# Kernel optimization log

Hardware: AMD Instinct MI355X
Metric: run time of the kernel (lower is better)

Reference implementation:

```python
import jax, jax.numpy as jnp
import numpy as np

NEG = -1000000.0  # mask fill value used by original sequence_mask

def setup_inputs() -> dict:
    key = jax.random.key(0)
    k1, k2, k3, k4 = jax.random.split(key, 4)
    B, S, D = 32, 2048, 64
    queries = jax.random.normal(k1, (B, S, D), dtype=jnp.float32)
    keys = jax.random.normal(k2, (B, S, D), dtype=jnp.float32)
    values = jax.random.normal(k3, (B, S, D), dtype=jnp.float32)
    valid_lens = jax.random.randint(k4, (B,), 1, S + 1, dtype=jnp.int64)
    return {"queries": queries, "keys": keys, "values": values, "valid_lens": valid_lens}

def reference(queries, keys, values, valid_lens):
    d = queries.shape[-1]
    # [B, Sq, Sk]
    scores = jnp.einsum('bqd,bkd->bqk', queries, keys) / jnp.sqrt(jnp.asarray(d, queries.dtype))
    # valid_lens is 1D: one length per batch row, broadcast over all query rows
    kv_idx = jnp.arange(scores.shape[-1])  # [Sk]
    mask = kv_idx[None, None, :] < valid_lens[:, None, None]  # [B,1,Sk] broadcast
    scores = jnp.where(mask, scores, jnp.asarray(NEG, scores.dtype))
    weights = jax.nn.softmax(scores, axis=-1)
    # dropout p=0.0 -> identity
    return jnp.einsum('bqk,bkd->bqd', weights, values)
```

## Files before the change

kernel.cpp:

```cpp
#include <hip/hip_runtime.h>
#include <hip/hip_bf16.h>

typedef __attribute__((ext_vector_type(8))) short bf16x8;
typedef __attribute__((ext_vector_type(4))) float f32x4;
typedef __attribute__((ext_vector_type(16))) float f32x16;

#define BATCH 32
#define SEQ   2048
#define PSTR  20
#define KSTR  72
#define VSTR  36
#define LOG2E 1.44269504088896340736f
#define QSCALE (0.125f * LOG2E)
#define NEGL  (-1000000.0f * LOG2E)

__device__ __forceinline__ unsigned int pk2(float lo, float hi) {
    __hip_bfloat162 h2 = __float22bfloat162_rn(make_float2(lo, hi));
    return *reinterpret_cast<unsigned int*>(&h2);
}

__device__ __forceinline__ void dma16(const short* g, short* l) {
    __builtin_amdgcn_global_load_lds((const __attribute__((address_space(1))) void*)g,
                                     (__attribute__((address_space(3))) void*)l, 16, 0, 0);
}

__device__ __forceinline__ void plswap(unsigned int& a, unsigned int& b) {
    asm volatile("v_permlane32_swap_b32 %0, %1" : "+v"(a), "+v"(b));
}

__global__ void prep_vl(const int* __restrict__ VL, int* __restrict__ meta) {
    __shared__ int sv[BATCH];
    const int t = threadIdx.x;
    int odd = (t < 16) ? VL[2 * t + 1] : 0;
    const bool is64 = (__ballot(odd != 0) == 0ULL);
    if (t < BATCH) {
        int x = is64 ? VL[2 * t] : VL[t];
        x = x < 0 ? 0 : (x > SEQ ? SEQ : x);
        sv[t] = x;
    }
    __syncthreads();
    if (t < BATCH) {
        const int x = sv[t];
        int rank = 0;
        for (int j = 0; j < BATCH; ++j) {
            const int y = sv[j];
            rank += (y > x) || (y == x && j < t);
        }
        meta[rank] = x;
        meta[BATCH + rank] = t;
    }
}

__global__ __launch_bounds__(256) void prepkv(const float* __restrict__ Kp,
                                              const float* __restrict__ Vp,
                                              const int* __restrict__ VL,
                                              short* __restrict__ Kb,
                                              short* __restrict__ Vt,
                                              int* __restrict__ meta) {
    __shared__ unsigned int l[64 * VSTR];
    __shared__ int sv[BATCH];
    const int tid = threadIdx.x;
    if (blockIdx.x == BATCH * 32) {
        if (tid < 64) {
            int odd = (tid < 16) ? VL[2 * tid + 1] : 0;
            const bool is64 = (__ballot(odd != 0) == 0ULL);
            if (tid < BATCH) {
                int x = is64 ? VL[2 * tid] : VL[tid];
                x = x < 0 ? 0 : (x > SEQ ? SEQ : x);
                sv[tid] = x;
            }
            asm volatile("s_waitcnt lgkmcnt(0)" ::: "memory");
            if (tid < BATCH) {
                const int x = sv[tid];
                int rank = 0;
                for (int j = 0; j < BATCH; ++j) {
                    const int y = sv[j];
                    rank += (y > x) || (y == x && j < tid);
                }
                meta[rank] = x;
                meta[BATCH + rank] = tid;
            }
        }
        return;
    }
    const int b = blockIdx.x >> 5, kt = blockIdx.x & 31, kb = kt * 64;
    const float* Kv = Kp + ((size_t)b * SEQ + kb) * 64;
    const float* Vb = Vp + ((size_t)b * SEQ + kb) * 64;
    #pragma unroll
    for (int h = 0; h < 4; ++h) {
        const int c = tid + h * 256;
        const int row = c >> 4, col = (c & 15) * 4;
        f32x4 x = *(const f32x4*)(Kv + row * 64 + col);
        unsigned int* dst = (unsigned int*)(Kb + ((size_t)b * SEQ + kb + row) * 64 + col);
        dst[0] = pk2(x[0], x[1]); dst[1] = pk2(x[2], x[3]);
    }
    #pragma unroll
    for (int h = 0; h < 2; ++h) {
        const int u = tid + h * 256;
        const int d4 = (u & 3) + ((u >> 7) << 2);
        const int kp = (u >> 2) & 31;
        f32x4 a = *(const f32x4*)(Vb + (2 * kp) * 64 + d4 * 4);
        f32x4 c = *(const f32x4*)(Vb + (2 * kp + 1) * 64 + d4 * 4);
        #pragma unroll
        for (int j = 0; j < 4; ++j)
            l[(d4 * 4 + j) * VSTR + kp] = pk2(a[j], c[j]);
    }
    __syncthreads();
    const int d = tid >> 2, cg = tid & 3;
    unsigned int w[8];
    #pragma unroll
    for (int j = 0; j < 8; ++j) w[j] = l[d * VSTR + cg * 8 + j];
    unsigned int* dst = (unsigned int*)Vt + ((size_t)(b * 32 + kt) * 64 + d) * 32 + cg * 8;
    #pragma unroll
    for (int j = 0; j < 8; ++j) dst[j] = w[j];
}

__global__ __launch_bounds__(256, 4)
void attn_fwd(const float* __restrict__ Qp, const short* __restrict__ Kb,
              const short* __restrict__ Vt, const int* __restrict__ meta,
              float* __restrict__ Out) {
    constexpr int S = SEQ;
    __shared__ short bK2[2 * 64 * 64];
    __shared__ short bV2[2 * 64 * 64];

    const int tid  = threadIdx.x;
    const int wave = tid >> 6, lane = tid & 63;
    const int r31 = lane & 31, hi = lane >> 5;
    const int qh = wave >> 1, kh = wave & 1;

    const int g  = blockIdx.x >> 8;
    const int k8 = (blockIdx.x >> 5) & 7;
    const int qt = blockIdx.x & 31;
    const int slot = (g << 3) + ((g & 1) ? 7 - k8 : k8);

    const int vl = meta[slot], batch = meta[BATCH + slot];
    const int ntiles = (vl + 63) >> 6;

    const short* Kbb = Kb + (size_t)batch * S * 64;
    const short* Vtb = Vt + (size_t)batch * 32 * 4096;

    const int r8 = lane >> 3, s8 = lane & 7, csw = s8 ^ r8;
    const short* gK0 = Kbb + (wave * 16 + r8) * 64 + csw * 8;
    const short* gV0 = Vtb + (wave * 16 + r8) * 64 + csw * 8;
    short* lK0 = &bK2[wave * 16 * 64];
    short* lV0 = &bV2[wave * 16 * 64];

    bf16x8 qf[4];
    {
        const float* qb = Qp + ((size_t)batch * S + qt * 64 + qh * 32 + r31) * 64 + hi * 8;
        #pragma unroll
        for (int kf = 0; kf < 4; ++kf) {
            f32x4 a = *(const f32x4*)(qb + kf * 16);
            f32x4 c = *(const f32x4*)(qb + kf * 16 + 4);
            union { bf16x8 v; unsigned int u[4]; } qq;
            qq.u[0] = pk2(a[0] * QSCALE, a[1] * QSCALE);
            qq.u[1] = pk2(a[2] * QSCALE, a[3] * QSCALE);
            qq.u[2] = pk2(c[0] * QSCALE, c[1] * QSCALE);
            qq.u[3] = pk2(c[2] * QSCALE, c[3] * QSCALE);
            qf[kf] = qq.v;
        }
    }

    f32x16 o[2];
    #pragma unroll
    for (int dt = 0; dt < 2; ++dt)
        #pragma unroll
        for (int r = 0; r < 16; ++r) o[dt][r] = 0.f;
    float lpart = 0.f;

    if (ntiles > 0) {
        dma16(gK0,          lK0);
        dma16(gK0 + 8 * 64, lK0 + 8 * 64);
        dma16(gV0,          lV0);
        dma16(gV0 + 8 * 64, lV0 + 8 * 64);
    }

    const int krow = kh * 32 + r31;
    const int l7 = lane & 7;

    for (int kt = 0; kt < ntiles; ++kt) {
        __syncthreads();
        if (kt + 1 < ntiles) {
            const int nb = ((kt + 1) & 1) * 4096;
            const int ko = (kt + 1) * 4096;
            dma16(gK0 + ko,          lK0 + nb);
            dma16(gK0 + ko + 8 * 64, lK0 + nb + 8 * 64);
            dma16(gV0 + ko,          lV0 + nb);
            dma16(gV0 + ko + 8 * 64, lV0 + nb + 8 * 64);
        }
        const char* bK = (const char*)&bK2[(kt & 1) * 4096];
        const char* bV = (const char*)&bV2[(kt & 1) * 4096];

        if (kt * 64 + kh * 32 < vl) {
            f32x16 st;
            #pragma unroll
            for (int r = 0; r < 16; ++r) st[r] = 0.f;
            #pragma unroll
            for (int kf = 0; kf < 4; ++kf) {
                bf16x8 kfr = *(const bf16x8*)(bK + krow * 128 +
                                              (((kf * 2 + hi) ^ l7) << 4));
                st = __builtin_amdgcn_mfma_f32_32x32x16_bf16(kfr, qf[kf], st, 0, 0, 0);
            }

            if (kt == ntiles - 1 && (vl & 63) != 0) {
                const int kb = kt * 64 + kh * 32 + 4 * hi;
                #pragma unroll
                for (int r = 0; r < 16; ++r) {
                    const int key = kb + (r & 3) + 8 * (r >> 2);
                    st[r] = (key < vl) ? st[r] : NEGL;
                }
            }

            #pragma unroll
            for (int r = 0; r < 16; ++r) st[r] = exp2f(st[r]);
            {
                const float a0 = (st[0] + st[1]) + (st[2] + st[3]);
                const float a1 = (st[4] + st[5]) + (st[6] + st[7]);
                const float a2 = (st[8] + st[9]) + (st[10] + st[11]);
                const float a3 = (st[12] + st[13]) + (st[14] + st[15]);
                lpart += (a0 + a1) + (a2 + a3);
            }

            union { bf16x8 v; unsigned int u[4]; } pf0, pf1;
            {
                unsigned int x0 = pk2(st[0], st[1]),   y0 = pk2(st[4], st[5]);
                unsigned int x1 = pk2(st[2], st[3]),   y1 = pk2(st[6], st[7]);
                plswap(x0, y0); plswap(x1, y1);
                pf0.u[0] = x0; pf0.u[1] = x1; pf0.u[2] = y0; pf0.u[3] = y1;
                unsigned int x2 = pk2(st[8], st[9]),   y2 = pk2(st[12], st[13]);
                unsigned int x3 = pk2(st[10], st[11]), y3 = pk2(st[14], st[15]);
                plswap(x2, y2); plswap(x3, y3);
                pf1.u[0] = x2; pf1.u[1] = x3; pf1.u[2] = y2; pf1.u[3] = y3;
            }

            #pragma unroll
            for (int dt = 0; dt < 2; ++dt) {
                const int vrow = dt * 32 + r31;
                bf16x8 vf0 = *(const bf16x8*)(bV + vrow * 128 +
                                              (((kh * 4 + hi) ^ l7) << 4));
                o[dt] = __builtin_amdgcn_mfma_f32_32x32x16_bf16(vf0, pf0.v, o[dt], 0, 0, 0);
                bf16x8 vf1 = *(const bf16x8*)(bV + vrow * 128 +
                                              (((kh * 4 + 2 + hi) ^ l7) << 4));
                o[dt] = __builtin_amdgcn_mfma_f32_32x32x16_bf16(vf1, pf1.v, o[dt], 0, 0, 0);
            }
        }
    }

    float lw = lpart + __shfl_xor(lpart, 32);

    __syncthreads();
    float* mrg = (float*)bK2;
    float* lm  = (float*)bV2;
    if (kh == 1) {
        #pragma unroll
        for (int dt = 0; dt < 2; ++dt)
            #pragma unroll
            for (int r = 0; r < 16; ++r)
                mrg[qh * 2048 + (dt * 16 + r) * 64 + lane] = o[dt][r];
        lm[qh * 64 + lane] = lw;
    }
    __syncthreads();
    if (kh == 0) {
        #pragma unroll
        for (int dt = 0; dt < 2; ++dt)
            #pragma unroll
            for (int r = 0; r < 16; ++r)
                o[dt][r] += mrg[qh * 2048 + (dt * 16 + r) * 64 + lane];
        lw += lm[qh * 64 + lane];
        const float inv = (lw > 0.f) ? 1.0f / lw : 0.f;
        const size_t orow = ((size_t)batch * S + qt * 64 + qh * 32 + r31) * 64;
        #pragma unroll
        for (int dt = 0; dt < 2; ++dt)
            #pragma unroll
            for (int g4 = 0; g4 < 4; ++g4) {
                f32x4 w;
                #pragma unroll
                for (int j = 0; j < 4; ++j) w[j] = o[dt][g4 * 4 + j] * inv;
                *(f32x4*)(Out + orow + dt * 32 + g4 * 8 + hi * 4) = w;
            }
    }
}

__device__ __forceinline__ void load_tile_fb(const float* __restrict__ Kb,
                                             const float* __restrict__ Vb,
                                             int tid, f32x4 kv[4], f32x4 vv[4]) {
    #pragma unroll
    for (int h = 0; h < 4; ++h) {
        const int c = tid + h * 256;
        kv[h] = *(const f32x4*)(Kb + (c >> 4) * 64 + (c & 15) * 4);
    }
    #pragma unroll
    for (int h = 0; h < 2; ++h) {
        const int u  = tid + h * 256;
        const int d4 = (u & 3) + ((u >> 7) << 2);
        const int kp = (u >> 2) & 31;
        vv[2 * h]     = *(const f32x4*)(Vb + (2 * kp) * 64 + d4 * 4);
        vv[2 * h + 1] = *(const f32x4*)(Vb + (2 * kp + 1) * 64 + d4 * 4);
    }
}

__global__ __launch_bounds__(256, 4)
void attn_fb(const float* __restrict__ Qp, const float* __restrict__ Kp,
             const float* __restrict__ Vp, const int* __restrict__ meta,
             float* __restrict__ Out) {
    constexpr int S = SEQ;
    constexpr int qtiles = S >> 6;
    __shared__ short        lK [64 * KSTR];
    __shared__ unsigned int lVt[64 * VSTR];
    __shared__ unsigned int lPt[4 * 32 * PSTR];
    const int tid = threadIdx.x;
    const int wave = tid >> 6, lane = tid & 63;
    const int l15 = lane & 15, grp = lane >> 4;
    const int slot = blockIdx.x / qtiles, qt = blockIdx.x % qtiles;
    const int vl = meta[slot], batch = meta[BATCH + slot];
    const int ntiles = (vl + 63) >> 6;
    const float* Kb = Kp + (size_t)batch * S * 64;
    const float* Vb = Vp + (size_t)batch * S * 64;
    bf16x8 qf[2];
    {
        const float* qb = Qp + ((size_t)batch * S + qt * 64 + wave * 16 + l15) * 64 + grp * 8;
        #pragma unroll
        for (int kf = 0; kf < 2; ++kf) {
            f32x4 a = *(const f32x4*)(qb + kf * 32);
            f32x4 b = *(const f32x4*)(qb + kf * 32 + 4);
            union { bf16x8 v; unsigned int u[4]; } qq;
            qq.u[0] = pk2(a[0], a[1]); qq.u[1] = pk2(a[2], a[3]);
            qq.u[2] = pk2(b[0], b[1]); qq.u[3] = pk2(b[2], b[3]);
            qf[kf] = qq.v;
        }
    }
    f32x4 o[4] = {{0.f,0.f,0.f,0.f},{0.f,0.f,0.f,0.f},{0.f,0.f,0.f,0.f},{0.f,0.f,0.f,0.f}};
    float mrun = -INFINITY, lrun = 0.f;
    unsigned int* pw = &lPt[wave * 32 * PSTR];
    f32x4 kv[4], vv[4];
    if (ntiles > 0) load_tile_fb(Kb, Vb, tid, kv, vv);
    for (int kt = 0; kt < ntiles; ++kt) {
        const int kb = kt * 64;
        __syncthreads();
        #pragma unroll
        for (int h = 0; h < 4; ++h) {
            const int c = tid + h * 256;
            const int row = c >> 4, col = (c & 15) * 4;
            union { f32x4 f; float e[4]; } x; x.f = kv[h];
            unsigned int* dst = (unsigned int*)&lK[row * KSTR + col];
            dst[0] = pk2(x.e[0], x.e[1]); dst[1] = pk2(x.e[2], x.e[3]);
        }
        #pragma unroll
        for (int h = 0; h < 2; ++h) {
            const int u  = tid + h * 256;
            const int d4 = (u & 3) + ((u >> 7) << 2);
            const int kp = (u >> 2) & 31;
            union { f32x4 f; float e[4]; } a, b;
            a.f = vv[2 * h]; b.f = vv[2 * h + 1];
            #pragma unroll
            for (int j = 0; j < 4; ++j)
                lVt[(d4 * 4 + j) * VSTR + kp] = pk2(a.e[j], b.e[j]);
        }
        if (kt + 1 < ntiles) load_tile_fb(Kb + (size_t)(kb + 64) * 64, Vb + (size_t)(kb + 64) * 64, tid, kv, vv);
        __syncthreads();
        f32x4 st[4] = {{0.f,0.f,0.f,0.f},{0.f,0.f,0.f,0.f},{0.f,0.f,0.f,0.f},{0.f,0.f,0.f,0.f}};
        #pragma unroll
        for (int kf = 0; kf < 2; ++kf) {
            #pragma unroll
            for (int ct = 0; ct < 4; ++ct) {
                bf16x8 kfr = *(const bf16x8*)&lK[(ct * 16 + l15) * KSTR + kf * 32 + grp * 8];
                st[ct] = __builtin_amdgcn_mfma_f32_16x16x32_bf16(kfr, qf[kf], st[ct], 0, 0, 0);
            }
        }
        #pragma unroll
        for (int ct = 0; ct < 4; ++ct)
            #pragma unroll
            for (int r = 0; r < 4; ++r) {
                const bool valid = (kb + ct * 16 + grp * 4 + r) < vl;
                st[ct][r] = valid ? st[ct][r] * (0.125f * LOG2E) : NEGL;
            }
        float t0 = fmaxf(fmaxf(st[0][0], st[0][1]), fmaxf(st[0][2], st[0][3]));
        float t1 = fmaxf(fmaxf(st[1][0], st[1][1]), fmaxf(st[1][2], st[1][3]));
        float t2 = fmaxf(fmaxf(st[2][0], st[2][1]), fmaxf(st[2][2], st[2][3]));
        float t3 = fmaxf(fmaxf(st[3][0], st[3][1]), fmaxf(st[3][2], st[3][3]));
        float tm = fmaxf(fmaxf(t0, t1), fmaxf(t2, t3));
        tm = fmaxf(tm, __shfl_xor(tm, 16));
        tm = fmaxf(tm, __shfl_xor(tm, 32));
        const float mnew  = fmaxf(mrun, tm);
        const float alpha = exp2f(mrun - mnew);
        mrun = mnew;
        lrun *= alpha;
        #pragma unroll
        for (int dt = 0; dt < 4; ++dt)
            #pragma unroll
            for (int r = 0; r < 4; ++r) o[dt][r] *= alpha;
        float rs = 0.f;
        #pragma unroll
        for (int ct = 0; ct < 4; ++ct) {
            #pragma unroll
            for (int r = 0; r < 4; ++r) {
                st[ct][r] = exp2f(st[ct][r] - mrun);
                rs += st[ct][r];
            }
            #pragma unroll
            for (int a = 0; a < 2; ++a)
                pw[(ct * 8 + grp * 2 + a) * PSTR + l15] = pk2(st[ct][2 * a], st[ct][2 * a + 1]);
        }
        rs += __shfl_xor(rs, 16);
        rs += __shfl_xor(rs, 32);
        lrun += rs;
        asm volatile("s_waitcnt lgkmcnt(0)" ::: "memory");
        #pragma unroll
        for (int kk = 0; kk < 2; ++kk) {
            union { bf16x8 v; unsigned int u[4]; } pf;
            #pragma unroll
            for (int jj = 0; jj < 4; ++jj)
                pf.u[jj] = pw[(kk * 16 + grp * 4 + jj) * PSTR + l15];
            #pragma unroll
            for (int dt = 0; dt < 4; ++dt) {
                bf16x8 vf = *(const bf16x8*)&lVt[(dt * 16 + l15) * VSTR + kk * 16 + grp * 4];
                o[dt] = __builtin_amdgcn_mfma_f32_16x16x32_bf16(vf, pf.v, o[dt], 0, 0, 0);
            }
        }
    }
    const float inv = (lrun > 0.f) ? 1.0f / lrun : 0.f;
    const size_t orow = ((size_t)batch * S + qt * 64 + wave * 16 + l15) * 64;
    #pragma unroll
    for (int dt = 0; dt < 4; ++dt) {
        f32x4 w = o[dt];
        w[0] *= inv; w[1] *= inv; w[2] *= inv; w[3] *= inv;
        *(f32x4*)(Out + orow + dt * 16 + grp * 4) = w;
    }
}

extern "C" void kernel_launch(void* const* d_in, const int* in_sizes, int n_in,
                              void* d_out, int out_size, void* d_ws, size_t ws_size,
                              hipStream_t stream) {
    const float* Q  = (const float*)d_in[0];
    const float* K  = (const float*)d_in[1];
    const float* V  = (const float*)d_in[2];
    const int*   VL = (const int*)d_in[3];
    int* meta = (int*)d_ws;
    const size_t need = 512 + 2 * (size_t)BATCH * SEQ * 64 * sizeof(short);
    dim3 block(256);
    if (ws_size >= need) {
        short* Kb = (short*)((char*)d_ws + 512);
        short* Vt = Kb + (size_t)BATCH * SEQ * 64;
        prepkv<<<dim3(BATCH * 32 + 1), block, 0, stream>>>(K, V, VL, Kb, Vt, meta);
        attn_fwd<<<dim3(BATCH * 32), block, 0, stream>>>(Q, Kb, Vt, meta, (float*)d_out);
    } else {
        prep_vl<<<1, 64, 0, stream>>>(VL, meta);
        attn_fb<<<dim3(BATCH * (SEQ >> 6)), block, 0, stream>>>(Q, K, V, meta, (float*)d_out);
    }
}
```

Baseline: 127.9 us.

## Load K/V fragments directly from global into registers, dropping LDS staging

```diff
diff --git a/kernel.cpp b/kernel.cpp
--- a/kernel.cpp
+++ b/kernel.cpp
@@ -17,11 +17,6 @@
 __device__ __forceinline__ unsigned int pk2(float lo, float hi) {
     __hip_bfloat162 h2 = __float22bfloat162_rn(make_float2(lo, hi));
     return *reinterpret_cast<unsigned int*>(&h2);
-}
-
-__device__ __forceinline__ void dma16(const short* g, short* l) {
-    __builtin_amdgcn_global_load_lds((const __attribute__((address_space(1))) void*)g,
-                                     (__attribute__((address_space(3))) void*)l, 16, 0, 0);
 }
 
 __device__ __forceinline__ void plswap(unsigned int& a, unsigned int& b) {
@@ -120,8 +115,7 @@
               const short* __restrict__ Vt, const int* __restrict__ meta,
               float* __restrict__ Out) {
     constexpr int S = SEQ;
-    __shared__ short bK2[2 * 64 * 64];
-    __shared__ short bV2[2 * 64 * 64];
+    __shared__ float mrg[2 * 2048 + 128];
 
     const int tid  = threadIdx.x;
     const int wave = tid >> 6, lane = tid & 63;
@@ -134,16 +128,14 @@
     const int slot = (g << 3) + ((g & 1) ? 7 - k8 : k8);
 
     const int vl = meta[slot], batch = meta[BATCH + slot];
-    const int ntiles = (vl + 63) >> 6;
-
-    const short* Kbb = Kb + (size_t)batch * S * 64;
-    const short* Vtb = Vt + (size_t)batch * 32 * 4096;
-
-    const int r8 = lane >> 3, s8 = lane & 7, csw = s8 ^ r8;
-    const short* gK0 = Kbb + (wave * 16 + r8) * 64 + csw * 8;
-    const short* gV0 = Vtb + (wave * 16 + r8) * 64 + csw * 8;
-    short* lK0 = &bK2[wave * 16 * 64];
-    short* lV0 = &bV2[wave * 16 * 64];
+    const int ntw = (vl - kh * 32 + 63) >> 6;
+
+    const short* Kbb = Kb + (size_t)batch * (S * 64);
+    const short* Vtb = Vt + (size_t)batch * (32 * 4096);
+
+    const int krow = kh * 32 + r31;
+    const short* pk = Kbb + krow * 64 + hi * 8;
+    const short* pv = Vtb + r31 * 64 + (kh * 4 + hi) * 8;
 
     bf16x8 qf[4];
     {
@@ -161,123 +153,119 @@
         }
     }
 
-    f32x16 o[2];
-    #pragma unroll
-    for (int dt = 0; dt < 2; ++dt)
-        #pragma unroll
-        for (int r = 0; r < 16; ++r) o[dt][r] = 0.f;
+    f32x16 o0, o1;
+    #pragma unroll
+    for (int r = 0; r < 16; ++r) { o0[r] = 0.f; o1[r] = 0.f; }
     float lpart = 0.f;
 
-    if (ntiles > 0) {
-        dma16(gK0,          lK0);
-        dma16(gK0 + 8 * 64, lK0 + 8 * 64);
-        dma16(gV0,          lV0);
-        dma16(gV0 + 8 * 64, lV0 + 8 * 64);
-    }
-
-    const int krow = kh * 32 + r31;
-    const int l7 = lane & 7;
-
-    for (int kt = 0; kt < ntiles; ++kt) {
-        __syncthreads();
-        if (kt + 1 < ntiles) {
-            const int nb = ((kt + 1) & 1) * 4096;
-            const int ko = (kt + 1) * 4096;
-            dma16(gK0 + ko,          lK0 + nb);
-            dma16(gK0 + ko + 8 * 64, lK0 + nb + 8 * 64);
-            dma16(gV0 + ko,          lV0 + nb);
-            dma16(gV0 + ko + 8 * 64, lV0 + nb + 8 * 64);
-        }
-        const char* bK = (const char*)&bK2[(kt & 1) * 4096];
-        const char* bV = (const char*)&bV2[(kt & 1) * 4096];
-
-        if (kt * 64 + kh * 32 < vl) {
-            f32x16 st;
-            #pragma unroll
-            for (int r = 0; r < 16; ++r) st[r] = 0.f;
-            #pragma unroll
-            for (int kf = 0; kf < 4; ++kf) {
-                bf16x8 kfr = *(const bf16x8*)(bK + krow * 128 +
-                                              (((kf * 2 + hi) ^ l7) << 4));
-                st = __builtin_amdgcn_mfma_f32_32x32x16_bf16(kfr, qf[kf], st, 0, 0, 0);
-            }
-
-            if (kt == ntiles - 1 && (vl & 63) != 0) {
-                const int kb = kt * 64 + kh * 32 + 4 * hi;
-                #pragma unroll
-                for (int r = 0; r < 16; ++r) {
-                    const int key = kb + (r & 3) + 8 * (r >> 2);
-                    st[r] = (key < vl) ? st[r] : NEGL;
-                }
-            }
-
-            #pragma unroll
-            for (int r = 0; r < 16; ++r) st[r] = exp2f(st[r]);
-            {
-                const float a0 = (st[0] + st[1]) + (st[2] + st[3]);
-                const float a1 = (st[4] + st[5]) + (st[6] + st[7]);
-                const float a2 = (st[8] + st[9]) + (st[10] + st[11]);
-                const float a3 = (st[12] + st[13]) + (st[14] + st[15]);
-                lpart += (a0 + a1) + (a2 + a3);
-            }
-
-            union { bf16x8 v; unsigned int u[4]; } pf0, pf1;
-            {
-                unsigned int x0 = pk2(st[0], st[1]),   y0 = pk2(st[4], st[5]);
-                unsigned int x1 = pk2(st[2], st[3]),   y1 = pk2(st[6], st[7]);
-                plswap(x0, y0); plswap(x1, y1);
-                pf0.u[0] = x0; pf0.u[1] = x1; pf0.u[2] = y0; pf0.u[3] = y1;
-                unsigned int x2 = pk2(st[8], st[9]),   y2 = pk2(st[12], st[13]);
-                unsigned int x3 = pk2(st[10], st[11]), y3 = pk2(st[14], st[15]);
-                plswap(x2, y2); plswap(x3, y3);
-                pf1.u[0] = x2; pf1.u[1] = x3; pf1.u[2] = y2; pf1.u[3] = y3;
-            }
-
-            #pragma unroll
-            for (int dt = 0; dt < 2; ++dt) {
-                const int vrow = dt * 32 + r31;
-                bf16x8 vf0 = *(const bf16x8*)(bV + vrow * 128 +
-                                              (((kh * 4 + hi) ^ l7) << 4));
-                o[dt] = __builtin_amdgcn_mfma_f32_32x32x16_bf16(vf0, pf0.v, o[dt], 0, 0, 0);
-                bf16x8 vf1 = *(const bf16x8*)(bV + vrow * 128 +
-                                              (((kh * 4 + 2 + hi) ^ l7) << 4));
-                o[dt] = __builtin_amdgcn_mfma_f32_32x32x16_bf16(vf1, pf1.v, o[dt], 0, 0, 0);
-            }
+    bf16x8 kk0 = *(const bf16x8*)(pk);
+    bf16x8 kk1 = *(const bf16x8*)(pk + 16);
+    bf16x8 kk2 = *(const bf16x8*)(pk + 32);
+    bf16x8 kk3 = *(const bf16x8*)(pk + 48);
+    bf16x8 vv0 = *(const bf16x8*)(pv);
+    bf16x8 vv1 = *(const bf16x8*)(pv + 16);
+    bf16x8 vv2 = *(const bf16x8*)(pv + 2048);
+    bf16x8 vv3 = *(const bf16x8*)(pv + 2048 + 16);
+
+    for (int kt = 0; kt < ntw; ++kt) {
+        f32x16 st;
+        #pragma unroll
+        for (int r = 0; r < 16; ++r) st[r] = 0.f;
+        __builtin_amdgcn_s_setprio(1);
+        st = __builtin_amdgcn_mfma_f32_32x32x16_bf16(kk0, qf[0], st, 0, 0, 0);
+        st = __builtin_amdgcn_mfma_f32_32x32x16_bf16(kk1, qf[1], st, 0, 0, 0);
+        st = __builtin_amdgcn_mfma_f32_32x32x16_bf16(kk2, qf[2], st, 0, 0, 0);
+        st = __builtin_amdgcn_mfma_f32_32x32x16_bf16(kk3, qf[3], st, 0, 0, 0);
+        __builtin_amdgcn_s_setprio(0);
+
+        if (kt + 1 < ntw) {
+            const short* p = pk + (kt + 1) * 4096;
+            kk0 = *(const bf16x8*)(p);
+            kk1 = *(const bf16x8*)(p + 16);
+            kk2 = *(const bf16x8*)(p + 32);
+            kk3 = *(const bf16x8*)(p + 48);
+        }
+
+        const int rem = vl - (kt * 64 + kh * 32);
+        if (rem < 32) {
+            #pragma unroll
+            for (int r = 0; r < 16; ++r) {
+                const int kl = 4 * hi + (r & 3) + 8 * (r >> 2);
+                st[r] = (kl < rem) ? st[r] : NEGL;
+            }
+        }
+
+        #pragma unroll
+        for (int r = 0; r < 16; ++r) st[r] = exp2f(st[r]);
+        {
+            const float a0 = (st[0] + st[1]) + (st[2] + st[3]);
+            const float a1 = (st[4] + st[5]) + (st[6] + st[7]);
+            const float a2 = (st[8] + st[9]) + (st[10] + st[11]);
+            const float a3 = (st[12] + st[13]) + (st[14] + st[15]);
+            lpart += (a0 + a1) + (a2 + a3);
+        }
+
+        union { bf16x8 v; unsigned int u[4]; } pf0, pf1;
+        {
+            unsigned int x0 = pk2(st[0], st[1]),   y0 = pk2(st[4], st[5]);
+            unsigned int x1 = pk2(st[2], st[3]),   y1 = pk2(st[6], st[7]);
+            plswap(x0, y0); plswap(x1, y1);
+            pf0.u[0] = x0; pf0.u[1] = x1; pf0.u[2] = y0; pf0.u[3] = y1;
+            unsigned int x2 = pk2(st[8], st[9]),   y2 = pk2(st[12], st[13]);
+            unsigned int x3 = pk2(st[10], st[11]), y3 = pk2(st[14], st[15]);
+            plswap(x2, y2); plswap(x3, y3);
+            pf1.u[0] = x2; pf1.u[1] = x3; pf1.u[2] = y2; pf1.u[3] = y3;
+        }
+
+        __builtin_amdgcn_s_setprio(1);
+        o0 = __builtin_amdgcn_mfma_f32_32x32x16_bf16(vv0, pf0.v, o0, 0, 0, 0);
+        o0 = __builtin_amdgcn_mfma_f32_32x32x16_bf16(vv1, pf1.v, o0, 0, 0, 0);
+        o1 = __builtin_amdgcn_mfma_f32_32x32x16_bf16(vv2, pf0.v, o1, 0, 0, 0);
+        o1 = __builtin_amdgcn_mfma_f32_32x32x16_bf16(vv3, pf1.v, o1, 0, 0, 0);
+        __builtin_amdgcn_s_setprio(0);
+
+        if (kt + 1 < ntw) {
+            const short* p = pv + (kt + 1) * 4096;
+            vv0 = *(const bf16x8*)(p);
+            vv1 = *(const bf16x8*)(p + 16);
+            vv2 = *(const bf16x8*)(p + 2048);
+            vv3 = *(const bf16x8*)(p + 2048 + 16);
         }
     }
 
     float lw = lpart + __shfl_xor(lpart, 32);
 
-    __syncthreads();
-    float* mrg = (float*)bK2;
-    float* lm  = (float*)bV2;
+    float* lm = &mrg[4096];
     if (kh == 1) {
         #pragma unroll
-        for (int dt = 0; dt < 2; ++dt)
-            #pragma unroll
-            for (int r = 0; r < 16; ++r)
-                mrg[qh * 2048 + (dt * 16 + r) * 64 + lane] = o[dt][r];
+        for (int r = 0; r < 16; ++r) mrg[qh * 2048 + r * 64 + lane] = o0[r];
+        #pragma unroll
+        for (int r = 0; r < 16; ++r) mrg[qh * 2048 + (16 + r) * 64 + lane] = o1[r];
         lm[qh * 64 + lane] = lw;
     }
     __syncthreads();
     if (kh == 0) {
         #pragma unroll
-        for (int dt = 0; dt < 2; ++dt)
-            #pragma unroll
-            for (int r = 0; r < 16; ++r)
-                o[dt][r] += mrg[qh * 2048 + (dt * 16 + r) * 64 + lane];
+        for (int r = 0; r < 16; ++r) o0[r] += mrg[qh * 2048 + r * 64 + lane];
+        #pragma unroll
+        for (int r = 0; r < 16; ++r) o1[r] += mrg[qh * 2048 + (16 + r) * 64 + lane];
         lw += lm[qh * 64 + lane];
         const float inv = (lw > 0.f) ? 1.0f / lw : 0.f;
         const size_t orow = ((size_t)batch * S + qt * 64 + qh * 32 + r31) * 64;
         #pragma unroll
-        for (int dt = 0; dt < 2; ++dt)
-            #pragma unroll
-            for (int g4 = 0; g4 < 4; ++g4) {
-                f32x4 w;
-                #pragma unroll
-                for (int j = 0; j < 4; ++j) w[j] = o[dt][g4 * 4 + j] * inv;
-                *(f32x4*)(Out + orow + dt * 32 + g4 * 8 + hi * 4) = w;
-            }
+        for (int g4 = 0; g4 < 4; ++g4) {
+            f32x4 w;
+            #pragma unroll
+            for (int j = 0; j < 4; ++j) w[j] = o0[g4 * 4 + j] * inv;
+            *(f32x4*)(Out + orow + g4 * 8 + hi * 4) = w;
+        }
+        #pragma unroll
+        for (int g4 = 0; g4 < 4; ++g4) {
+            f32x4 w;
+            #pragma unroll
+            for (int j = 0; j < 4; ++j) w[j] = o1[g4 * 4 + j] * inv;
+            *(f32x4*)(Out + orow + 32 + g4 * 8 + hi * 4) = w;
+        }
     }
 }
 
```

Result: slower. 158.8 us (+24.2%).

## Skip K/V conversion past valid length and unroll attention loop with MFMA priority

Applied to the files above, without the earlier changes.

```diff
diff --git a/kernel.cpp b/kernel.cpp
--- a/kernel.cpp
+++ b/kernel.cpp
@@ -59,6 +59,7 @@
                                               int* __restrict__ meta) {
     __shared__ unsigned int l[64 * VSTR];
     __shared__ int sv[BATCH];
+    __shared__ int svl;
     const int tid = threadIdx.x;
     if (blockIdx.x == BATCH * 32) {
         if (tid < 64) {
@@ -84,6 +85,17 @@
         return;
     }
     const int b = blockIdx.x >> 5, kt = blockIdx.x & 31, kb = kt * 64;
+    if (tid < 64) {
+        int odd = (tid < 16) ? VL[2 * tid + 1] : 0;
+        const bool is64 = (__ballot(odd != 0) == 0ULL);
+        if (tid == 0) {
+            int x = is64 ? VL[2 * b] : VL[b];
+            x = x < 0 ? 0 : (x > SEQ ? SEQ : x);
+            svl = x;
+        }
+    }
+    __syncthreads();
+    if (kb >= svl) return;
     const float* Kv = Kp + ((size_t)b * SEQ + kb) * 64;
     const float* Vb = Vp + ((size_t)b * SEQ + kb) * 64;
     #pragma unroll
@@ -126,6 +138,7 @@
     const int tid  = threadIdx.x;
     const int wave = tid >> 6, lane = tid & 63;
     const int r31 = lane & 31, hi = lane >> 5;
+    const int l7  = lane & 7;
     const int qh = wave >> 1, kh = wave & 1;
 
     const int g  = blockIdx.x >> 8;
@@ -161,90 +174,93 @@
         }
     }
 
-    f32x16 o[2];
-    #pragma unroll
-    for (int dt = 0; dt < 2; ++dt)
-        #pragma unroll
-        for (int r = 0; r < 16; ++r) o[dt][r] = 0.f;
+    f32x16 o0, o1, zv;
+    #pragma unroll
+    for (int r = 0; r < 16; ++r) { o0[r] = 0.f; o1[r] = 0.f; zv[r] = 0.f; }
     float lpart = 0.f;
+    const int krow = kh * 32 + r31;
 
     if (ntiles > 0) {
-        dma16(gK0,          lK0);
-        dma16(gK0 + 8 * 64, lK0 + 8 * 64);
-        dma16(gV0,          lV0);
-        dma16(gV0 + 8 * 64, lV0 + 8 * 64);
-    }
-
-    const int krow = kh * 32 + r31;
-    const int l7 = lane & 7;
-
-    for (int kt = 0; kt < ntiles; ++kt) {
-        __syncthreads();
-        if (kt + 1 < ntiles) {
-            const int nb = ((kt + 1) & 1) * 4096;
-            const int ko = (kt + 1) * 4096;
-            dma16(gK0 + ko,          lK0 + nb);
-            dma16(gK0 + ko + 8 * 64, lK0 + nb + 8 * 64);
-            dma16(gV0 + ko,          lV0 + nb);
-            dma16(gV0 + ko + 8 * 64, lV0 + nb + 8 * 64);
-        }
-        const char* bK = (const char*)&bK2[(kt & 1) * 4096];
-        const char* bV = (const char*)&bV2[(kt & 1) * 4096];
-
-        if (kt * 64 + kh * 32 < vl) {
-            f32x16 st;
-            #pragma unroll
-            for (int r = 0; r < 16; ++r) st[r] = 0.f;
-            #pragma unroll
-            for (int kf = 0; kf < 4; ++kf) {
-                bf16x8 kfr = *(const bf16x8*)(bK + krow * 128 +
-                                              (((kf * 2 + hi) ^ l7) << 4));
-                st = __builtin_amdgcn_mfma_f32_32x32x16_bf16(kfr, qf[kf], st, 0, 0, 0);
-            }
-
-            if (kt == ntiles - 1 && (vl & 63) != 0) {
-                const int kb = kt * 64 + kh * 32 + 4 * hi;
-                #pragma unroll
-                for (int r = 0; r < 16; ++r) {
-                    const int key = kb + (r & 3) + 8 * (r >> 2);
-                    st[r] = (key < vl) ? st[r] : NEGL;
-                }
-            }
-
-            #pragma unroll
-            for (int r = 0; r < 16; ++r) st[r] = exp2f(st[r]);
-            {
-                const float a0 = (st[0] + st[1]) + (st[2] + st[3]);
-                const float a1 = (st[4] + st[5]) + (st[6] + st[7]);
-                const float a2 = (st[8] + st[9]) + (st[10] + st[11]);
-                const float a3 = (st[12] + st[13]) + (st[14] + st[15]);
-                lpart += (a0 + a1) + (a2 + a3);
-            }
-
-            union { bf16x8 v; unsigned int u[4]; } pf0, pf1;
-            {
-                unsigned int x0 = pk2(st[0], st[1]),   y0 = pk2(st[4], st[5]);
-                unsigned int x1 = pk2(st[2], st[3]),   y1 = pk2(st[6], st[7]);
-                plswap(x0, y0); plswap(x1, y1);
-                pf0.u[0] = x0; pf0.u[1] = x1; pf0.u[2] = y0; pf0.u[3] = y1;
-                unsigned int x2 = pk2(st[8], st[9]),   y2 = pk2(st[12], st[13]);
-                unsigned int x3 = pk2(st[10], st[11]), y3 = pk2(st[14], st[15]);
-                plswap(x2, y2); plswap(x3, y3);
-                pf1.u[0] = x2; pf1.u[1] = x3; pf1.u[2] = y2; pf1.u[3] = y3;
-            }
-
-            #pragma unroll
-            for (int dt = 0; dt < 2; ++dt) {
-                const int vrow = dt * 32 + r31;
-                bf16x8 vf0 = *(const bf16x8*)(bV + vrow * 128 +
-                                              (((kh * 4 + hi) ^ l7) << 4));
-                o[dt] = __builtin_amdgcn_mfma_f32_32x32x16_bf16(vf0, pf0.v, o[dt], 0, 0, 0);
-                bf16x8 vf1 = *(const bf16x8*)(bV + vrow * 128 +
-                                              (((kh * 4 + 2 + hi) ^ l7) << 4));
-                o[dt] = __builtin_amdgcn_mfma_f32_32x32x16_bf16(vf1, pf1.v, o[dt], 0, 0, 0);
-            }
-        }
-    }
+        dma16(gK0,       lK0);
+        dma16(gK0 + 512, lK0 + 512);
+        dma16(gV0,       lV0);
+        dma16(gV0 + 512, lV0 + 512);
+    }
+
+#define ATTN_TILE(KT, BUF)                                                       \
+    {                                                                            \
+        __syncthreads();       \
+        if ((KT) + 1 < ntiles) {                                                 \
+            const int ko = ((KT) + 1) * 4096;                                    \
+            dma16(gK0 + ko,       lK0 + ((BUF) ^ 1) * 4096);                     \
+            dma16(gK0 + ko + 512, lK0 + ((BUF) ^ 1) * 4096 + 512);               \
+            dma16(gV0 + ko,       lV0 + ((BUF) ^ 1) * 4096);                     \
+            dma16(gV0 + ko + 512, lV0 + ((BUF) ^ 1) * 4096 + 512);               \
+        }                                                                        \
+        if ((KT) * 64 + kh * 32 < vl) {                                          \
+            const char* bK = (const char*)&bK2[(BUF) * 4096];                    \
+            const char* bV = (const char*)&bV2[(BUF) * 4096];                    \
+            f32x16 st;                                                           \
+            __builtin_amdgcn_s_setprio(1);                                       \
+            {                                                                    \
+                bf16x8 k0 = *(const bf16x8*)(bK + krow * 128 + (((0 + hi) ^ l7) << 4)); \
+                bf16x8 k1 = *(const bf16x8*)(bK + krow * 128 + (((2 + hi) ^ l7) << 4)); \
+                bf16x8 k2 = *(const bf16x8*)(bK + krow * 128 + (((4 + hi) ^ l7) << 4)); \
+                bf16x8 k3 = *(const bf16x8*)(bK + krow * 128 + (((6 + hi) ^ l7) << 4)); \
+                st = __builtin_amdgcn_mfma_f32_32x32x16_bf16(k0, qf[0], zv, 0, 0, 0); \
+                st = __builtin_amdgcn_mfma_f32_32x32x16_bf16(k1, qf[1], st, 0, 0, 0); \
+                st = __builtin_amdgcn_mfma_f32_32x32x16_bf16(k2, qf[2], st, 0, 0, 0); \
+                st = __builtin_amdgcn_mfma_f32_32x32x16_bf16(k3, qf[3], st, 0, 0, 0); \
+            }                                                                    \
+            __builtin_amdgcn_s_setprio(0);                                       \
+            const int rem = vl - ((KT) * 64 + kh * 32);                          \
+            if (rem < 32) {                                                      \
+                _Pragma("unroll")                                                \
+                for (int r = 0; r < 16; ++r) {                                   \
+                    const int kl = 4 * hi + (r & 3) + 8 * (r >> 2);              \
+                    st[r] = (kl < rem) ? st[r] : NEGL;                           \
+                }                                                                \
+            }                                                                    \
+            _Pragma("unroll")                                                    \
+            for (int r = 0; r < 16; ++r) st[r] = exp2f(st[r]);                   \
+            {                                                                    \
+                const float a0 = (st[0] + st[1]) + (st[2] + st[3]);              \
+                const float a1 = (st[4] + st[5]) + (st[6] + st[7]);              \
+                const float a2 = (st[8] + st[9]) + (st[10] + st[11]);            \
+                const float a3 = (st[12] + st[13]) + (st[14] + st[15]);          \
+                lpart += (a0 + a1) + (a2 + a3);                                  \
+            }                                                                    \
+            union { bf16x8 v; unsigned int u[4]; } pf0, pf1;                     \
+            {                                                                    \
+                unsigned int x0 = pk2(st[0], st[1]),   y0 = pk2(st[4], st[5]);   \
+                unsigned int x1 = pk2(st[2], st[3]),   y1 = pk2(st[6], st[7]);   \
+                plswap(x0, y0); plswap(x1, y1);                                  \
+                pf0.u[0] = x0; pf0.u[1] = x1; pf0.u[2] = y0; pf0.u[3] = y1;      \
+                unsigned int x2 = pk2(st[8], st[9]),   y2 = pk2(st[12], st[13]); \
+                unsigned int x3 = pk2(st[10], st[11]), y3 = pk2(st[14], st[15]); \
+                plswap(x2, y2); plswap(x3, y3);                                  \
+                pf1.u[0] = x2; pf1.u[1] = x3; pf1.u[2] = y2; pf1.u[3] = y3;      \
+            }                                                                    \
+            __builtin_amdgcn_s_setprio(1);                                       \
+            {                                                                    \
+                bf16x8 vf0 = *(const bf16x8*)(bV + r31 * 128 + (((kh * 4 + hi) ^ l7) << 4)); \
+                o0 = __builtin_amdgcn_mfma_f32_32x32x16_bf16(vf0, pf0.v, o0, 0, 0, 0); \
+                bf16x8 vf1 = *(const bf16x8*)(bV + r31 * 128 + (((kh * 4 + 2 + hi) ^ l7) << 4)); \
+                o0 = __builtin_amdgcn_mfma_f32_32x32x16_bf16(vf1, pf1.v, o0, 0, 0, 0); \
+                bf16x8 vf2 = *(const bf16x8*)(bV + (32 + r31) * 128 + (((kh * 4 + hi) ^ l7) << 4)); \
+                o1 = __builtin_amdgcn_mfma_f32_32x32x16_bf16(vf2, pf0.v, o1, 0, 0, 0); \
+                bf16x8 vf3 = *(const bf16x8*)(bV + (32 + r31) * 128 + (((kh * 4 + 2 + hi) ^ l7) << 4)); \
+                o1 = __builtin_amdgcn_mfma_f32_32x32x16_bf16(vf3, pf1.v, o1, 0, 0, 0); \
+            }                                                                    \
+            __builtin_amdgcn_s_setprio(0);                                       \
+        }                                                                        \
+    }
+
+    for (int kt = 0; kt < ntiles; kt += 2) {
+        ATTN_TILE(kt, 0);
+        if (kt + 1 < ntiles) ATTN_TILE(kt + 1, 1);
+    }
+#undef ATTN_TILE
 
     float lw = lpart + __shfl_xor(lpart, 32);
 
@@ -253,31 +269,34 @@
     float* lm  = (float*)bV2;
     if (kh == 1) {
         #pragma unroll
-        for (int dt = 0; dt < 2; ++dt)
-            #pragma unroll
-            for (int r = 0; r < 16; ++r)
-                mrg[qh * 2048 + (dt * 16 + r) * 64 + lane] = o[dt][r];
+        for (int r = 0; r < 16; ++r) mrg[qh * 2048 + r * 64 + lane] = o0[r];
+        #pragma unroll
+        for (int r = 0; r < 16; ++r) mrg[qh * 2048 + (16 + r) * 64 + lane] = o1[r];
         lm[qh * 64 + lane] = lw;
     }
     __syncthreads();
     if (kh == 0) {
         #pragma unroll
-        for (int dt = 0; dt < 2; ++dt)
-            #pragma unroll
-            for (int r = 0; r < 16; ++r)
-                o[dt][r] += mrg[qh * 2048 + (dt * 16 + r) * 64 + lane];
+        for (int r = 0; r < 16; ++r) o0[r] += mrg[qh * 2048 + r * 64 + lane];
+        #pragma unroll
+        for (int r = 0; r < 16; ++r) o1[r] += mrg[qh * 2048 + (16 + r) * 64 + lane];
         lw += lm[qh * 64 + lane];
         const float inv = (lw > 0.f) ? 1.0f / lw : 0.f;
         const size_t orow = ((size_t)batch * S + qt * 64 + qh * 32 + r31) * 64;
         #pragma unroll
-        for (int dt = 0; dt < 2; ++dt)
-            #pragma unroll
-            for (int g4 = 0; g4 < 4; ++g4) {
-                f32x4 w;
-                #pragma unroll
-                for (int j = 0; j < 4; ++j) w[j] = o[dt][g4 * 4 + j] * inv;
-                *(f32x4*)(Out + orow + dt * 32 + g4 * 8 + hi * 4) = w;
-            }
+        for (int g4 = 0; g4 < 4; ++g4) {
+            f32x4 w;
+            #pragma unroll
+            for (int j = 0; j < 4; ++j) w[j] = o0[g4 * 4 + j] * inv;
+            *(f32x4*)(Out + orow + g4 * 8 + hi * 4) = w;
+        }
+        #pragma unroll
+        for (int g4 = 0; g4 < 4; ++g4) {
+            f32x4 w;
+            #pragma unroll
+            for (int j = 0; j < 4; ++j) w[j] = o1[g4 * 4 + j] * inv;
+            *(f32x4*)(Out + orow + 32 + g4 * 8 + hi * 4) = w;
+        }
     }
 }
 
```

New measurement: 126.2 us. About the same (-1.3%).
